# Kernel tuning notes

Hardware: AMD Instinct MI355X
Metric: run time of the kernel (lower is better)

## Reference

```python
import jax, jax.numpy as jnp
import numpy as np

N = 50000      # nodes
E = 800000     # edges
F = 256        # input features (glove identity)
H = 64         # hidden dim of GCN stack
C = 16         # num classes
PE = 200000    # pos/neg edges each

@jax.custom_vjp
def grad_reverse(x):
    return x

def _gr_fwd(x):
    return x, None

def _gr_bwd(_, g):
    return (-g,)

grad_reverse.defvjp(_gr_fwd, _gr_bwd)

def _gcn_norm(edge_index, n):
    # add self loops + symmetric normalization (PyG GCNConv default)
    loops = jnp.arange(n, dtype=edge_index.dtype)
    src = jnp.concatenate([edge_index[0], loops])
    dst = jnp.concatenate([edge_index[1], loops])
    deg = jax.ops.segment_sum(jnp.ones(src.shape, jnp.float32), dst, num_segments=n)
    dinv = jnp.where(deg > 0, jax.lax.rsqrt(jnp.maximum(deg, 1.0)), 0.0)
    return src, dst, dinv[src] * dinv[dst]

def _gcn(x, W, b, src, dst, norm, n):
    h = x @ W                                   # [n, out]
    msg = h[src] * norm[:, None]                # gather + edge scale
    return jax.ops.segment_sum(msg, dst, num_segments=n) + b

def setup_inputs():
    key = jax.random.key(0)
    ks = jax.random.split(key, 14)
    s = 0.05
    return {
        "input": jax.random.normal(ks[0], (N, F), jnp.float32),
        "glove": jnp.eye(F, dtype=jnp.float32),
        "W1": jax.random.normal(ks[1], (F, H), jnp.float32) * s,
        "b1": jnp.zeros((H,), jnp.float32),
        "W2": jax.random.normal(ks[2], (H, H), jnp.float32) * s,
        "b2": jnp.zeros((H,), jnp.float32),
        "W3": jax.random.normal(ks[3], (H, H), jnp.float32) * s,
        "b3": jnp.zeros((H,), jnp.float32),
        "Wa": jax.random.normal(ks[4], (H, C), jnp.float32) * s,
        "ba": jnp.zeros((C,), jnp.float32),
        "Wk": jax.random.normal(ks[5], (H, C), jnp.float32) * s,
        "bk": jnp.zeros((C,), jnp.float32),
        "edge_index": jax.random.randint(ks[6], (2, E), 0, N, dtype=jnp.int32),
        "pos_edge_index": jax.random.randint(ks[7], (2, PE), 0, N, dtype=jnp.int32),
        "neg_edge_index": jax.random.randint(ks[8], (2, PE), 0, N, dtype=jnp.int32),
    }

def reference(input, glove, W1, b1, W2, b2, W3, b3, Wa, ba, Wk, bk,
              edge_index, pos_edge_index, neg_edge_index):
    src, dst, norm = _gcn_norm(edge_index, N)
    x = input @ glove
    x = jax.nn.relu(_gcn(x, W1, b1, src, dst, norm, N))
    x = _gcn(x, W2, b2, src, dst, norm, N)
    x = _gcn(x, W3, b3, src, dst, norm, N)
    feat = x
    attr = _gcn(x, Wa, ba, src, dst, norm, N)
    att = _gcn(grad_reverse(x), Wk, bk, src, dst, norm, N)
    tei = jnp.concatenate([pos_edge_index, neg_edge_index], axis=-1)  # [2, 2*PE]
    x_j = x[tei[0]]
    x_i = x[tei[1]]
    res = jnp.einsum('ef,ef->e', x_i, x_j)
    return res, jax.nn.log_softmax(attr, axis=1), att, feat
```

## Files before the change

### kernel.cpp

```cpp
#include <hip/hip_runtime.h>
#include <hip/hip_bf16.h>

#define N_NODES 50000
#define N_EDGES 800000
#define F_IN    256
#define H_DIM   64
#define C_DIM   16
#define PE_CNT  200000

typedef __hip_bfloat16 bf16;

__device__ __forceinline__ float b2f(bf16 v) { return __bfloat162float(v); }
__device__ __forceinline__ bf16  f2b(float v) { return __float2bfloat16(v); }
__device__ __forceinline__ unsigned short f2b_u(float v) {
    union { bf16 b; unsigned short u; } cv; cv.b = __float2bfloat16(v); return cv.u;
}


__global__ void hist_build_kernel(const int* __restrict__ dst, int* __restrict__ hist,
                                  const float* __restrict__ Wa, const float* __restrict__ Wk,
                                  float* __restrict__ Wh) {
    int e = blockIdx.x * blockDim.x + threadIdx.x;
    if (e < N_EDGES) atomicAdd(&hist[dst[e]], 1);
    if (blockIdx.x == 0) {
        for (int idx = threadIdx.x; idx < H_DIM * 32; idx += 256) {
            int f = idx >> 5, c = idx & 31;
            Wh[idx] = (c < C_DIM) ? Wa[f * C_DIM + c] : Wk[f * C_DIM + (c - C_DIM)];
        }
    }
}

__global__ __launch_bounds__(1024) void scan_block_kernel(const int* __restrict__ hist,
                                                          int* __restrict__ excl,
                                                          int* __restrict__ partials) {
    __shared__ int buf[1024];
    int i = blockIdx.x * 1024 + threadIdx.x;
    int v = (i < N_NODES) ? hist[i] : 0;
    buf[threadIdx.x] = v;
    __syncthreads();
    for (int off = 1; off < 1024; off <<= 1) {
        int t = (threadIdx.x >= off) ? buf[threadIdx.x - off] : 0;
        __syncthreads();
        buf[threadIdx.x] += t;
        __syncthreads();
    }
    int incl = buf[threadIdx.x];
    if (i < N_NODES) excl[i] = incl - v;
    if (threadIdx.x == 1023) partials[blockIdx.x] = incl;
}

__global__ void scan_partials_kernel(int* __restrict__ partials) {
    int t = threadIdx.x;
    int orig = (t < 49) ? partials[t] : 0;
    int v = orig;
    for (int off = 1; off < 64; off <<= 1) {
        int u = __shfl_up(v, off, 64);
        if (t >= off) v += u;
    }
    if (t < 49) partials[t] = v - orig;
}

__global__ void scan_add_kernel(int* __restrict__ rowstart, const int* __restrict__ partials,
                                int* __restrict__ cursor, const int* __restrict__ hist,
                                float* __restrict__ dinv) {
    int i = blockIdx.x * blockDim.x + threadIdx.x;
    if (i < N_NODES) {
        int v = rowstart[i] + partials[i >> 10];
        rowstart[i] = v;
        cursor[i]   = v;
        dinv[i]     = rsqrtf((float)(hist[i] + 1));
    } else if (i == N_NODES) {
        rowstart[i] = N_EDGES;
    }
}

__global__ void scatter_kernel(const int* __restrict__ ei, int* __restrict__ cursor,
                               const float* __restrict__ dinv, int2* __restrict__ csr2) {
    int e = blockIdx.x * blockDim.x + threadIdx.x;
    if (e < N_EDGES) {
        int s = ei[e];
        int d = ei[N_EDGES + e];
        int p = atomicAdd(&cursor[d], 1);
        csr2[p] = make_int2(s, __float_as_int(dinv[s]));
    }
}

#define AGG_BODY(TBL, STRIDE, CIDX)                                                      \
    float acc0 = dn * b2f(TBL[(size_t)node * STRIDE + CIDX]);                            \
    float acc1 = 0.f, acc2 = 0.f, acc3 = 0.f;                                            \
    int j = s0;                                                                          \
    if ((j & 1) && j < s1) {                                                             \
        int2 e = csr2[j];                                                                \
        acc1 += __int_as_float(e.y) * b2f(TBL[(size_t)e.x * STRIDE + CIDX]);             \
        j++;                                                                             \
    }                                                                                    \
    for (; j + 3 < s1; j += 4) {                                                         \
        int4 p01 = *(const int4*)&csr2[j];                                               \
        int4 p23 = *(const int4*)&csr2[j + 2];                                           \
        acc0 += __int_as_float(p01.y) * b2f(TBL[(size_t)p01.x * STRIDE + CIDX]);         \
        acc1 += __int_as_float(p01.w) * b2f(TBL[(size_t)p01.z * STRIDE + CIDX]);         \
        acc2 += __int_as_float(p23.y) * b2f(TBL[(size_t)p23.x * STRIDE + CIDX]);         \
        acc3 += __int_as_float(p23.w) * b2f(TBL[(size_t)p23.z * STRIDE + CIDX]);         \
    }                                                                                    \
    for (; j < s1; j++) {                                                                \
        int2 e = csr2[j];                                                                \
        acc0 += __int_as_float(e.y) * b2f(TBL[(size_t)e.x * STRIDE + CIDX]);             \
    }                                                                                    \
    float aggsum = (acc0 + acc1) + (acc2 + acc3);

#define G_ROWS 32
#define G_KCH  64
#define XS_LD  68

__global__ __launch_bounds__(256) void gemm_k256_kernel(const float* __restrict__ x,
                                                        const float* __restrict__ W,
                                                        bf16* __restrict__ h1) {
    __shared__ float xs[G_ROWS * XS_LD];
    __shared__ float ws[G_KCH * H_DIM];
    int t = threadIdx.x;
    int row0 = blockIdx.x * G_ROWS;
    int c4 = (t & 15) * 4;
    int r2 = (t >> 4) * 2;

    float acc00 = 0.f, acc01 = 0.f, acc02 = 0.f, acc03 = 0.f;
    float acc10 = 0.f, acc11 = 0.f, acc12 = 0.f, acc13 = 0.f;

    for (int c = 0; c < F_IN / G_KCH; c++) {
        int k0 = c * G_KCH;
        {
            const float4* Wg = (const float4*)(W + k0 * H_DIM);
            float4* wl = (float4*)ws;
#pragma unroll
            for (int i = 0; i < 4; i++) wl[t + 256 * i] = Wg[t + 256 * i];
        }
        {
            int r = t >> 3, jj = (t & 7) * 8;
            int row = row0 + r;
            float4 v0 = make_float4(0.f, 0.f, 0.f, 0.f), v1 = v0;
            if (row < N_NODES) {
                const float4* xg = (const float4*)(x + (size_t)row * F_IN + k0 + jj);
                v0 = xg[0];
                v1 = xg[1];
            }
            float4* xl = (float4*)&xs[r * XS_LD + jj];
            xl[0] = v0;
            xl[1] = v1;
        }
        __syncthreads();
#pragma unroll 8
        for (int kk = 0; kk < G_KCH; kk += 4) {
            float4 xv0 = *(const float4*)&xs[(r2 + 0) * XS_LD + kk];
            float4 xv1 = *(const float4*)&xs[(r2 + 1) * XS_LD + kk];
            float4 w0 = *(const float4*)&ws[(kk + 0) * H_DIM + c4];
            float4 w1 = *(const float4*)&ws[(kk + 1) * H_DIM + c4];
            float4 w2 = *(const float4*)&ws[(kk + 2) * H_DIM + c4];
            float4 w3 = *(const float4*)&ws[(kk + 3) * H_DIM + c4];
            acc00 += xv0.x * w0.x + xv0.y * w1.x + xv0.z * w2.x + xv0.w * w3.x;
            acc01 += xv0.x * w0.y + xv0.y * w1.y + xv0.z * w2.y + xv0.w * w3.y;
            acc02 += xv0.x * w0.z + xv0.y * w1.z + xv0.z * w2.z + xv0.w * w3.z;
            acc03 += xv0.x * w0.w + xv0.y * w1.w + xv0.z * w2.w + xv0.w * w3.w;
            acc10 += xv1.x * w0.x + xv1.y * w1.x + xv1.z * w2.x + xv1.w * w3.x;
            acc11 += xv1.x * w0.y + xv1.y * w1.y + xv1.z * w2.y + xv1.w * w3.y;
            acc12 += xv1.x * w0.z + xv1.y * w1.z + xv1.z * w2.z + xv1.w * w3.z;
            acc13 += xv1.x * w0.w + xv1.y * w1.w + xv1.z * w2.w + xv1.w * w3.w;
        }
        __syncthreads();
    }
    int rowA = row0 + r2, rowB = rowA + 1;
    if (rowA < N_NODES) {
        ushort4 p = make_ushort4(f2b_u(acc00), f2b_u(acc01), f2b_u(acc02), f2b_u(acc03));
        *(ushort4*)&h1[(size_t)rowA * H_DIM + c4] = p;
    }
    if (rowB < N_NODES) {
        ushort4 p = make_ushort4(f2b_u(acc10), f2b_u(acc11), f2b_u(acc12), f2b_u(acc13));
        *(ushort4*)&h1[(size_t)rowB * H_DIM + c4] = p;
    }
}

template <int RELU>
__global__ __launch_bounds__(256) void agg_gemm_kernel(const bf16* __restrict__ h,
                                                       const int* __restrict__ rowstart,
                                                       const int2* __restrict__ csr2,
                                                       const float* __restrict__ dinv,
                                                       const float* __restrict__ bagg,
                                                       const float* __restrict__ W,
                                                       bf16* __restrict__ hnext) {
    __shared__ float Wl[H_DIM * H_DIM];
    int t = threadIdx.x;
    {
        const float4* Wg = (const float4*)W;
        float4* wl = (float4*)Wl;
#pragma unroll
        for (int i = 0; i < 4; i++) wl[t + 256 * i] = Wg[t + 256 * i];
    }
    __syncthreads();
    int lane = t & 63;
    int node = blockIdx.x * 4 + __builtin_amdgcn_readfirstlane(t >> 6);
    float dn = dinv[node];
    int s0 = rowstart[node], s1 = rowstart[node + 1];
    AGG_BODY(h, H_DIM, lane)
    float v = dn * aggsum + bagg[lane];
    if (RELU) v = fmaxf(v, 0.f);
    float o = 0.f;
#pragma unroll
    for (int f = 0; f < H_DIM; f++)
        o += __shfl(v, f, 64) * Wl[f * H_DIM + lane];
    hnext[(size_t)node * H_DIM + lane] = f2b(o);
}

__global__ __launch_bounds__(256) void agg_out_kernel(const bf16* __restrict__ h,
                                                      const int* __restrict__ rowstart,
                                                      const int2* __restrict__ csr2,
                                                      const float* __restrict__ dinv,
                                                      const float* __restrict__ b3,
                                                      const float* __restrict__ Wh,
                                                      float* __restrict__ feat,
                                                      bf16* __restrict__ featb,
                                                      bf16* __restrict__ zb) {
    __shared__ float Whs[H_DIM * 32];
    int t = threadIdx.x;
    {
        const float4* Wg = (const float4*)Wh;
        float4* wl = (float4*)Whs;
#pragma unroll
        for (int i = 0; i < 2; i++) wl[t + 256 * i] = Wg[t + 256 * i];
    }
    __syncthreads();
    int lane = t & 63;
    int node = blockIdx.x * 4 + __builtin_amdgcn_readfirstlane(t >> 6);
    float dn = dinv[node];
    int s0 = rowstart[node], s1 = rowstart[node + 1];
    AGG_BODY(h, H_DIM, lane)
    float v = dn * aggsum + b3[lane];
    feat[(size_t)node * H_DIM + lane]  = v;
    featb[(size_t)node * H_DIM + lane] = f2b(v);
    int c32 = lane & 31;
    float zc = 0.f;
#pragma unroll
    for (int f = 0; f < H_DIM; f++)
        zc += __shfl(v, f, 64) * Whs[f * 32 + c32];
    if (lane < 32) zb[(size_t)node * 32 + lane] = f2b(zc);
}

__global__ __launch_bounds__(256) void head_kernel(const bf16* __restrict__ zb,
                                                   const int* __restrict__ rowstart,
                                                   const int2* __restrict__ csr2,
                                                   const float* __restrict__ dinv,
                                                   const float* __restrict__ ba,
                                                   const float* __restrict__ bk,
                                                   float* __restrict__ lsm,
                                                   float* __restrict__ att) {
    int t = threadIdx.x;
    int lane = t & 63;
    int half = lane >> 5;
    int c32 = lane & 31;
    int wid = __builtin_amdgcn_readfirstlane(t >> 6);
    int node = blockIdx.x * 8 + wid * 2 + half;
    float dn = dinv[node];
    int s0 = rowstart[node], s1 = rowstart[node + 1];
    AGG_BODY(zb, 32, c32)
    float y = dn * aggsum;
    int c = c32 & 15;
    float hv = y + ((c32 < 16) ? ba[c] : bk[c]);
    if (c32 < 16) {
        float m = hv;
#pragma unroll
        for (int off = 1; off < 16; off <<= 1) m = fmaxf(m, __shfl_xor(m, off, 64));
        float e = __expf(hv - m);
        float sum = e;
#pragma unroll
        for (int off = 1; off < 16; off <<= 1) sum += __shfl_xor(sum, off, 64);
        lsm[(size_t)node * C_DIM + c] = (hv - m) - __logf(sum);
    } else {
        att[(size_t)node * C_DIM + c] = hv;
    }
}

__global__ __launch_bounds__(256) void edge_dot_kernel(const int* __restrict__ pos,
                                                       const int* __restrict__ neg,
                                                       const bf16* __restrict__ xb,
                                                       float* __restrict__ res) {
    int e = blockIdx.x * 32 + (threadIdx.x >> 3);
    int lane8 = threadIdx.x & 7;
    int a, b;
    if (e < PE_CNT) {
        a = pos[e];
        b = pos[PE_CNT + e];
    } else {
        int e2 = e - PE_CNT;
        a = neg[e2];
        b = neg[PE_CNT + e2];
    }
    uint4 ua = ((const uint4*)(xb + (size_t)a * H_DIM))[lane8];
    uint4 ub = ((const uint4*)(xb + (size_t)b * H_DIM))[lane8];
    float acc;
    {
        float s = 0.f;
        unsigned au, bu;
        au = ua.x; bu = ub.x;
        s += __uint_as_float(au << 16) * __uint_as_float(bu << 16);
        s += __uint_as_float(au & 0xffff0000u) * __uint_as_float(bu & 0xffff0000u);
        au = ua.y; bu = ub.y;
        s += __uint_as_float(au << 16) * __uint_as_float(bu << 16);
        s += __uint_as_float(au & 0xffff0000u) * __uint_as_float(bu & 0xffff0000u);
        au = ua.z; bu = ub.z;
        s += __uint_as_float(au << 16) * __uint_as_float(bu << 16);
        s += __uint_as_float(au & 0xffff0000u) * __uint_as_float(bu & 0xffff0000u);
        au = ua.w; bu = ub.w;
        s += __uint_as_float(au << 16) * __uint_as_float(bu << 16);
        s += __uint_as_float(au & 0xffff0000u) * __uint_as_float(bu & 0xffff0000u);
        acc = s;
    }
#pragma unroll
    for (int off = 1; off < 8; off <<= 1) acc += __shfl_xor(acc, off, 64);
    if (lane8 == 0) res[e] = acc;
}


extern "C" void kernel_launch(void* const* d_in, const int* in_sizes, int n_in,
                              void* d_out, int out_size, void* d_ws, size_t ws_size,
                              hipStream_t stream) {
    const float* input = (const float*)d_in[0];
    const float* W1 = (const float*)d_in[2];
    const float* b1 = (const float*)d_in[3];
    const float* W2 = (const float*)d_in[4];
    const float* b2 = (const float*)d_in[5];
    const float* W3 = (const float*)d_in[6];
    const float* b3 = (const float*)d_in[7];
    const float* Wa = (const float*)d_in[8];
    const float* ba = (const float*)d_in[9];
    const float* Wk = (const float*)d_in[10];
    const float* bk = (const float*)d_in[11];
    const int* ei  = (const int*)d_in[12];
    const int* pos = (const int*)d_in[13];
    const int* neg = (const int*)d_in[14];

    char* ws = (char*)d_ws;
    int*   hist     = (int*)(ws + 0);
    int*   rowstart = (int*)(ws + 200704);
    int*   cursor   = (int*)(ws + 401408);
    float* dinv     = (float*)(ws + 602112);
    int*   partials = (int*)(ws + 802816);
    float* Wh       = (float*)(ws + 803072);
    int2*  csr2     = (int2*)(ws + 811264);
    bf16*  bufA     = (bf16*)(ws + 7211264ULL);
    bf16*  bufB     = (bf16*)(ws + 13611264ULL);
    bf16*  zb       = (bf16*)(ws + 20011264ULL);

    float* out  = (float*)d_out;
    float* res  = out;
    float* lsm  = out + 400000;
    float* att  = out + 1200000;
    float* feat = out + 2000000;

    hipMemsetAsync(hist, 0, N_NODES * sizeof(int), stream);
    hist_build_kernel<<<(N_EDGES + 255) / 256, 256, 0, stream>>>(ei + N_EDGES, hist, Wa, Wk, Wh);
    scan_block_kernel<<<49, 1024, 0, stream>>>(hist, rowstart, partials);
    scan_partials_kernel<<<1, 64, 0, stream>>>(partials);
    scan_add_kernel<<<196, 256, 0, stream>>>(rowstart, partials, cursor, hist, dinv);
    scatter_kernel<<<(N_EDGES + 255) / 256, 256, 0, stream>>>(ei, cursor, dinv, csr2);

    gemm_k256_kernel<<<(N_NODES + G_ROWS - 1) / G_ROWS, 256, 0, stream>>>(input, W1, bufA);
    agg_gemm_kernel<1><<<12500, 256, 0, stream>>>(bufA, rowstart, csr2, dinv, b1, W2, bufB);
    agg_gemm_kernel<0><<<12500, 256, 0, stream>>>(bufB, rowstart, csr2, dinv, b2, W3, bufA);
    agg_out_kernel<<<12500, 256, 0, stream>>>(bufA, rowstart, csr2, dinv, b3, Wh, feat, bufB, zb);
    head_kernel<<<6250, 256, 0, stream>>>(zb, rowstart, csr2, dinv, ba, bk, lsm, att);
    edge_dot_kernel<<<12500, 256, 0, stream>>>(pos, neg, bufB, res);
}
```

Measured before the change: 459.0 us.

## Split CSR by source half to shrink gather working sets for L2 locality

Edges in each destination row are partitioned by source node (low or high half), and each aggregation becomes two passes. The first pass gathers only from the low half of the feature table into an fp32 accumulator buffer, and the second gathers from the high half and finishes the GEMM/epilogue. The edge-dot stage is also split into two passes over 32-column half tables, and the first GEMM uses 64-row tiles. The aim is to keep each pass's random-gather footprint cache resident, at the cost of extra kernel launches, an fp32 partial-sum round trip through memory, and a second read-modify-write of res.

```diff
diff --git a/kernel.cpp b/kernel.cpp
--- a/kernel.cpp
+++ b/kernel.cpp
@@ -2,6 +2,7 @@
 #include <hip/hip_bf16.h>
 
 #define N_NODES 50000
+#define N_HALF  25000
 #define N_EDGES 800000
 #define F_IN    256
 #define H_DIM   64
@@ -17,11 +18,17 @@
 }
 
 
-__global__ void hist_build_kernel(const int* __restrict__ dst, int* __restrict__ hist,
+__global__ void hist_build_kernel(const int* __restrict__ ei, int* __restrict__ hist_tot,
+                                  int* __restrict__ hist_lo,
                                   const float* __restrict__ Wa, const float* __restrict__ Wk,
                                   float* __restrict__ Wh) {
     int e = blockIdx.x * blockDim.x + threadIdx.x;
-    if (e < N_EDGES) atomicAdd(&hist[dst[e]], 1);
+    if (e < N_EDGES) {
+        int s = ei[e];
+        int d = ei[N_EDGES + e];
+        atomicAdd(&hist_tot[d], 1);
+        if (s < N_HALF) atomicAdd(&hist_lo[d], 1);
+    }
     if (blockIdx.x == 0) {
         for (int idx = threadIdx.x; idx < H_DIM * 32; idx += 256) {
             int f = idx >> 5, c = idx & 31;
@@ -61,40 +68,45 @@
 }
 
 __global__ void scan_add_kernel(int* __restrict__ rowstart, const int* __restrict__ partials,
-                                int* __restrict__ cursor, const int* __restrict__ hist,
+                                int* __restrict__ cursorA, int* __restrict__ split,
+                                int* __restrict__ cursorB,
+                                const int* __restrict__ hist_tot, const int* __restrict__ hist_lo,
                                 float* __restrict__ dinv) {
     int i = blockIdx.x * blockDim.x + threadIdx.x;
     if (i < N_NODES) {
         int v = rowstart[i] + partials[i >> 10];
         rowstart[i] = v;
-        cursor[i]   = v;
-        dinv[i]     = rsqrtf((float)(hist[i] + 1));
+        cursorA[i]  = v;
+        int sp = v + hist_lo[i];
+        split[i]    = sp;
+        cursorB[i]  = sp;
+        dinv[i]     = rsqrtf((float)(hist_tot[i] + 1));
     } else if (i == N_NODES) {
         rowstart[i] = N_EDGES;
     }
 }
 
-__global__ void scatter_kernel(const int* __restrict__ ei, int* __restrict__ cursor,
-                               const float* __restrict__ dinv, int2* __restrict__ csr2) {
+__global__ void scatter_kernel(const int* __restrict__ ei, int* __restrict__ cursorA,
+                               int* __restrict__ cursorB, const float* __restrict__ dinv,
+                               int2* __restrict__ csr2) {
     int e = blockIdx.x * blockDim.x + threadIdx.x;
     if (e < N_EDGES) {
         int s = ei[e];
         int d = ei[N_EDGES + e];
-        int p = atomicAdd(&cursor[d], 1);
+        int p = (s < N_HALF) ? atomicAdd(&cursorA[d], 1) : atomicAdd(&cursorB[d], 1);
         csr2[p] = make_int2(s, __float_as_int(dinv[s]));
     }
 }
 
-#define AGG_BODY(TBL, STRIDE, CIDX)                                                      \
-    float acc0 = dn * b2f(TBL[(size_t)node * STRIDE + CIDX]);                            \
+#define AGG_LOOP(TBL, STRIDE, CIDX, J0, J1)                                              \
     float acc1 = 0.f, acc2 = 0.f, acc3 = 0.f;                                            \
-    int j = s0;                                                                          \
-    if ((j & 1) && j < s1) {                                                             \
+    int j = (J0);                                                                        \
+    if ((j & 1) && j < (J1)) {                                                           \
         int2 e = csr2[j];                                                                \
         acc1 += __int_as_float(e.y) * b2f(TBL[(size_t)e.x * STRIDE + CIDX]);             \
         j++;                                                                             \
     }                                                                                    \
-    for (; j + 3 < s1; j += 4) {                                                         \
+    for (; j + 3 < (J1); j += 4) {                                                       \
         int4 p01 = *(const int4*)&csr2[j];                                               \
         int4 p23 = *(const int4*)&csr2[j + 2];                                           \
         acc0 += __int_as_float(p01.y) * b2f(TBL[(size_t)p01.x * STRIDE + CIDX]);         \
@@ -102,13 +114,13 @@
         acc2 += __int_as_float(p23.y) * b2f(TBL[(size_t)p23.x * STRIDE + CIDX]);         \
         acc3 += __int_as_float(p23.w) * b2f(TBL[(size_t)p23.z * STRIDE + CIDX]);         \
     }                                                                                    \
-    for (; j < s1; j++) {                                                                \
+    for (; j < (J1); j++) {                                                              \
         int2 e = csr2[j];                                                                \
         acc0 += __int_as_float(e.y) * b2f(TBL[(size_t)e.x * STRIDE + CIDX]);             \
     }                                                                                    \
     float aggsum = (acc0 + acc1) + (acc2 + acc3);
 
-#define G_ROWS 32
+#define G_ROWS 64
 #define G_KCH  64
 #define XS_LD  68
 
@@ -120,10 +132,13 @@
     int t = threadIdx.x;
     int row0 = blockIdx.x * G_ROWS;
     int c4 = (t & 15) * 4;
-    int r2 = (t >> 4) * 2;
-
-    float acc00 = 0.f, acc01 = 0.f, acc02 = 0.f, acc03 = 0.f;
-    float acc10 = 0.f, acc11 = 0.f, acc12 = 0.f, acc13 = 0.f;
+    int r4 = (t >> 4) * 4;
+
+    float acc[4][4];
+#pragma unroll
+    for (int i = 0; i < 4; i++)
+#pragma unroll
+        for (int q = 0; q < 4; q++) acc[i][q] = 0.f;
 
     for (int c = 0; c < F_IN / G_KCH; c++) {
         int k0 = c * G_KCH;
@@ -134,57 +149,70 @@
             for (int i = 0; i < 4; i++) wl[t + 256 * i] = Wg[t + 256 * i];
         }
         {
-            int r = t >> 3, jj = (t & 7) * 8;
+            int r = t >> 2, jj = (t & 3) * 16;
             int row = row0 + r;
-            float4 v0 = make_float4(0.f, 0.f, 0.f, 0.f), v1 = v0;
+            float4 v0 = make_float4(0.f, 0.f, 0.f, 0.f), v1 = v0, v2 = v0, v3 = v0;
             if (row < N_NODES) {
                 const float4* xg = (const float4*)(x + (size_t)row * F_IN + k0 + jj);
-                v0 = xg[0];
-                v1 = xg[1];
+                v0 = xg[0]; v1 = xg[1]; v2 = xg[2]; v3 = xg[3];
             }
             float4* xl = (float4*)&xs[r * XS_LD + jj];
-            xl[0] = v0;
-            xl[1] = v1;
+            xl[0] = v0; xl[1] = v1; xl[2] = v2; xl[3] = v3;
         }
         __syncthreads();
-#pragma unroll 8
+#pragma unroll 4
         for (int kk = 0; kk < G_KCH; kk += 4) {
-            float4 xv0 = *(const float4*)&xs[(r2 + 0) * XS_LD + kk];
-            float4 xv1 = *(const float4*)&xs[(r2 + 1) * XS_LD + kk];
-            float4 w0 = *(const float4*)&ws[(kk + 0) * H_DIM + c4];
-            float4 w1 = *(const float4*)&ws[(kk + 1) * H_DIM + c4];
-            float4 w2 = *(const float4*)&ws[(kk + 2) * H_DIM + c4];
-            float4 w3 = *(const float4*)&ws[(kk + 3) * H_DIM + c4];
-            acc00 += xv0.x * w0.x + xv0.y * w1.x + xv0.z * w2.x + xv0.w * w3.x;
-            acc01 += xv0.x * w0.y + xv0.y * w1.y + xv0.z * w2.y + xv0.w * w3.y;
-            acc02 += xv0.x * w0.z + xv0.y * w1.z + xv0.z * w2.z + xv0.w * w3.z;
-            acc03 += xv0.x * w0.w + xv0.y * w1.w + xv0.z * w2.w + xv0.w * w3.w;
-            acc10 += xv1.x * w0.x + xv1.y * w1.x + xv1.z * w2.x + xv1.w * w3.x;
-            acc11 += xv1.x * w0.y + xv1.y * w1.y + xv1.z * w2.y + xv1.w * w3.y;
-            acc12 += xv1.x * w0.z + xv1.y * w1.z + xv1.z * w2.z + xv1.w * w3.z;
-            acc13 += xv1.x * w0.w + xv1.y * w1.w + xv1.z * w2.w + xv1.w * w3.w;
+            float4 xv[4], wv[4];
+#pragma unroll
+            for (int i = 0; i < 4; i++) xv[i] = *(const float4*)&xs[(r4 + i) * XS_LD + kk];
+#pragma unroll
+            for (int q = 0; q < 4; q++) wv[q] = *(const float4*)&ws[(kk + q) * H_DIM + c4];
+#pragma unroll
+            for (int i = 0; i < 4; i++) {
+                acc[i][0] += xv[i].x * wv[0].x + xv[i].y * wv[1].x + xv[i].z * wv[2].x + xv[i].w * wv[3].x;
+                acc[i][1] += xv[i].x * wv[0].y + xv[i].y * wv[1].y + xv[i].z * wv[2].y + xv[i].w * wv[3].y;
+                acc[i][2] += xv[i].x * wv[0].z + xv[i].y * wv[1].z + xv[i].z * wv[2].z + xv[i].w * wv[3].z;
+                acc[i][3] += xv[i].x * wv[0].w + xv[i].y * wv[1].w + xv[i].z * wv[2].w + xv[i].w * wv[3].w;
+            }
         }
         __syncthreads();
     }
-    int rowA = row0 + r2, rowB = rowA + 1;
-    if (rowA < N_NODES) {
-        ushort4 p = make_ushort4(f2b_u(acc00), f2b_u(acc01), f2b_u(acc02), f2b_u(acc03));
-        *(ushort4*)&h1[(size_t)rowA * H_DIM + c4] = p;
-    }
-    if (rowB < N_NODES) {
-        ushort4 p = make_ushort4(f2b_u(acc10), f2b_u(acc11), f2b_u(acc12), f2b_u(acc13));
-        *(ushort4*)&h1[(size_t)rowB * H_DIM + c4] = p;
-    }
+#pragma unroll
+    for (int i = 0; i < 4; i++) {
+        int row = row0 + r4 + i;
+        if (row < N_NODES) {
+            ushort4 p = make_ushort4(f2b_u(acc[i][0]), f2b_u(acc[i][1]),
+                                     f2b_u(acc[i][2]), f2b_u(acc[i][3]));
+            *(ushort4*)&h1[(size_t)row * H_DIM + c4] = p;
+        }
+    }
+}
+
+__global__ __launch_bounds__(256) void aggA_kernel(const bf16* __restrict__ h,
+                                                   const int* __restrict__ rowstart,
+                                                   const int* __restrict__ split,
+                                                   const int2* __restrict__ csr2,
+                                                   const float* __restrict__ dinv,
+                                                   float* __restrict__ accbuf) {
+    int lane = threadIdx.x & 63;
+    int node = blockIdx.x * 4 + __builtin_amdgcn_readfirstlane(threadIdx.x >> 6);
+    float dn = dinv[node];
+    int s0 = rowstart[node], s1 = split[node];
+    float acc0 = (node < N_HALF) ? dn * b2f(h[(size_t)node * H_DIM + lane]) : 0.f;
+    AGG_LOOP(h, H_DIM, lane, s0, s1)
+    __builtin_nontemporal_store(aggsum, &accbuf[(size_t)node * H_DIM + lane]);
 }
 
 template <int RELU>
-__global__ __launch_bounds__(256) void agg_gemm_kernel(const bf16* __restrict__ h,
-                                                       const int* __restrict__ rowstart,
-                                                       const int2* __restrict__ csr2,
-                                                       const float* __restrict__ dinv,
-                                                       const float* __restrict__ bagg,
-                                                       const float* __restrict__ W,
-                                                       bf16* __restrict__ hnext) {
+__global__ __launch_bounds__(256) void aggB_gemm_kernel(const bf16* __restrict__ h,
+                                                        const int* __restrict__ rowstart,
+                                                        const int* __restrict__ split,
+                                                        const int2* __restrict__ csr2,
+                                                        const float* __restrict__ dinv,
+                                                        const float* __restrict__ accbuf,
+                                                        const float* __restrict__ bagg,
+                                                        const float* __restrict__ W,
+                                                        bf16* __restrict__ hnext) {
     __shared__ float Wl[H_DIM * H_DIM];
     int t = threadIdx.x;
     {
@@ -197,8 +225,10 @@
     int lane = t & 63;
     int node = blockIdx.x * 4 + __builtin_amdgcn_readfirstlane(t >> 6);
     float dn = dinv[node];
-    int s0 = rowstart[node], s1 = rowstart[node + 1];
-    AGG_BODY(h, H_DIM, lane)
+    int s0 = split[node], s1 = rowstart[node + 1];
+    float acc0 = __builtin_nontemporal_load(&accbuf[(size_t)node * H_DIM + lane]);
+    if (node >= N_HALF) acc0 += dn * b2f(h[(size_t)node * H_DIM + lane]);
+    AGG_LOOP(h, H_DIM, lane, s0, s1)
     float v = dn * aggsum + bagg[lane];
     if (RELU) v = fmaxf(v, 0.f);
     float o = 0.f;
@@ -208,15 +238,18 @@
     hnext[(size_t)node * H_DIM + lane] = f2b(o);
 }
 
-__global__ __launch_bounds__(256) void agg_out_kernel(const bf16* __restrict__ h,
-                                                      const int* __restrict__ rowstart,
-                                                      const int2* __restrict__ csr2,
-                                                      const float* __restrict__ dinv,
-                                                      const float* __restrict__ b3,
-                                                      const float* __restrict__ Wh,
-                                                      float* __restrict__ feat,
-                                                      bf16* __restrict__ featb,
-                                                      bf16* __restrict__ zb) {
+__global__ __launch_bounds__(256) void aggB_out_kernel(const bf16* __restrict__ h,
+                                                       const int* __restrict__ rowstart,
+                                                       const int* __restrict__ split,
+                                                       const int2* __restrict__ csr2,
+                                                       const float* __restrict__ dinv,
+                                                       const float* __restrict__ accbuf,
+                                                       const float* __restrict__ b3,
+                                                       const float* __restrict__ Wh,
+                                                       float* __restrict__ feat,
+                                                       bf16* __restrict__ featL,
+                                                       bf16* __restrict__ featH,
+                                                       bf16* __restrict__ zb) {
     __shared__ float Whs[H_DIM * 32];
     int t = threadIdx.x;
     {
@@ -229,12 +262,15 @@
     int lane = t & 63;
     int node = blockIdx.x * 4 + __builtin_amdgcn_readfirstlane(t >> 6);
     float dn = dinv[node];
-    int s0 = rowstart[node], s1 = rowstart[node + 1];
-    AGG_BODY(h, H_DIM, lane)
+    int s0 = split[node], s1 = rowstart[node + 1];
+    float acc0 = __builtin_nontemporal_load(&accbuf[(size_t)node * H_DIM + lane]);
+    if (node >= N_HALF) acc0 += dn * b2f(h[(size_t)node * H_DIM + lane]);
+    AGG_LOOP(h, H_DIM, lane, s0, s1)
     float v = dn * aggsum + b3[lane];
-    feat[(size_t)node * H_DIM + lane]  = v;
-    featb[(size_t)node * H_DIM + lane] = f2b(v);
+    feat[(size_t)node * H_DIM + lane] = v;
     int c32 = lane & 31;
+    bf16* half_tbl = (lane >= 32) ? featH : featL;
+    half_tbl[(size_t)node * 32 + c32] = f2b(v);
     float zc = 0.f;
 #pragma unroll
     for (int f = 0; f < H_DIM; f++)
@@ -258,7 +294,8 @@
     int node = blockIdx.x * 8 + wid * 2 + half;
     float dn = dinv[node];
     int s0 = rowstart[node], s1 = rowstart[node + 1];
-    AGG_BODY(zb, 32, c32)
+    float acc0 = dn * b2f(zb[(size_t)node * 32 + c32]);
+    AGG_LOOP(zb, 32, c32, s0, s1)
     float y = dn * aggsum;
     int c = c32 & 15;
     float hv = y + ((c32 < 16) ? ba[c] : bk[c]);
@@ -278,10 +315,11 @@
 
 __global__ __launch_bounds__(256) void edge_dot_kernel(const int* __restrict__ pos,
                                                        const int* __restrict__ neg,
-                                                       const bf16* __restrict__ xb,
-                                                       float* __restrict__ res) {
-    int e = blockIdx.x * 32 + (threadIdx.x >> 3);
-    int lane8 = threadIdx.x & 7;
+                                                       const bf16* __restrict__ tbl,
+                                                       float* __restrict__ res,
+                                                       int accumulate) {
+    int e = blockIdx.x * 64 + (threadIdx.x >> 2);
+    int lane4 = threadIdx.x & 3;
     int a, b;
     if (e < PE_CNT) {
         a = pos[e];
@@ -291,29 +329,28 @@
         a = neg[e2];
         b = neg[PE_CNT + e2];
     }
-    uint4 ua = ((const uint4*)(xb + (size_t)a * H_DIM))[lane8];
-    uint4 ub = ((const uint4*)(xb + (size_t)b * H_DIM))[lane8];
-    float acc;
-    {
-        float s = 0.f;
-        unsigned au, bu;
-        au = ua.x; bu = ub.x;
-        s += __uint_as_float(au << 16) * __uint_as_float(bu << 16);
-        s += __uint_as_float(au & 0xffff0000u) * __uint_as_float(bu & 0xffff0000u);
-        au = ua.y; bu = ub.y;
-        s += __uint_as_float(au << 16) * __uint_as_float(bu << 16);
-        s += __uint_as_float(au & 0xffff0000u) * __uint_as_float(bu & 0xffff0000u);
-        au = ua.z; bu = ub.z;
-        s += __uint_as_float(au << 16) * __uint_as_float(bu << 16);
-        s += __uint_as_float(au & 0xffff0000u) * __uint_as_float(bu & 0xffff0000u);
-        au = ua.w; bu = ub.w;
-        s += __uint_as_float(au << 16) * __uint_as_float(bu << 16);
-        s += __uint_as_float(au & 0xffff0000u) * __uint_as_float(bu & 0xffff0000u);
-        acc = s;
-    }
-#pragma unroll
-    for (int off = 1; off < 8; off <<= 1) acc += __shfl_xor(acc, off, 64);
-    if (lane8 == 0) res[e] = acc;
+    uint4 ua = ((const uint4*)(tbl + (size_t)a * 32))[lane4];
+    uint4 ub = ((const uint4*)(tbl + (size_t)b * 32))[lane4];
+    float s = 0.f;
+    unsigned au, bu;
+    au = ua.x; bu = ub.x;
+    s += __uint_as_float(au << 16) * __uint_as_float(bu << 16);
+    s += __uint_as_float(au & 0xffff0000u) * __uint_as_float(bu & 0xffff0000u);
+    au = ua.y; bu = ub.y;
+    s += __uint_as_float(au << 16) * __uint_as_float(bu << 16);
+    s += __uint_as_float(au & 0xffff0000u) * __uint_as_float(bu & 0xffff0000u);
+    au = ua.z; bu = ub.z;
+    s += __uint_as_float(au << 16) * __uint_as_float(bu << 16);
+    s += __uint_as_float(au & 0xffff0000u) * __uint_as_float(bu & 0xffff0000u);
+    au = ua.w; bu = ub.w;
+    s += __uint_as_float(au << 16) * __uint_as_float(bu << 16);
+    s += __uint_as_float(au & 0xffff0000u) * __uint_as_float(bu & 0xffff0000u);
+#pragma unroll
+    for (int off = 1; off < 4; off <<= 1) s += __shfl_xor(s, off, 64);
+    if (lane4 == 0) {
+        if (accumulate) res[e] += s;
+        else            res[e]  = s;
+    }
 }
 
 
@@ -336,16 +373,22 @@
     const int* neg = (const int*)d_in[14];
 
     char* ws = (char*)d_ws;
-    int*   hist     = (int*)(ws + 0);
-    int*   rowstart = (int*)(ws + 200704);
-    int*   cursor   = (int*)(ws + 401408);
-    float* dinv     = (float*)(ws + 602112);
-    int*   partials = (int*)(ws + 802816);
-    float* Wh       = (float*)(ws + 803072);
-    int2*  csr2     = (int2*)(ws + 811264);
-    bf16*  bufA     = (bf16*)(ws + 7211264ULL);
-    bf16*  bufB     = (bf16*)(ws + 13611264ULL);
-    bf16*  zb       = (bf16*)(ws + 20011264ULL);
+    int*   hist_tot = (int*)(ws + 0);
+    int*   hist_lo  = (int*)(ws + 200704);
+    int*   rowstart = (int*)(ws + 401408);
+    int*   cursorA  = (int*)(ws + 602112);
+    int*   split    = (int*)(ws + 802816);
+    int*   cursorB  = (int*)(ws + 1003520);
+    float* dinv     = (float*)(ws + 1204224);
+    int*   partials = (int*)(ws + 1404928);
+    float* Wh       = (float*)(ws + 1405184);
+    int2*  csr2     = (int2*)(ws + 1413376);
+    bf16*  bufA     = (bf16*)(ws + 7813376ULL);
+    bf16*  bufB     = (bf16*)(ws + 14213376ULL);
+    bf16*  zb       = (bf16*)(ws + 20613376ULL);
+    bf16*  featL    = (bf16*)(ws + 23813376ULL);
+    bf16*  featH    = (bf16*)(ws + 27013376ULL);
+    float* accbuf   = (float*)(ws + 30213376ULL);
 
     float* out  = (float*)d_out;
     float* res  = out;
@@ -353,17 +396,26 @@
     float* att  = out + 1200000;
     float* feat = out + 2000000;
 
-    hipMemsetAsync(hist, 0, N_NODES * sizeof(int), stream);
-    hist_build_kernel<<<(N_EDGES + 255) / 256, 256, 0, stream>>>(ei + N_EDGES, hist, Wa, Wk, Wh);
-    scan_block_kernel<<<49, 1024, 0, stream>>>(hist, rowstart, partials);
+    hipMemsetAsync(hist_tot, 0, 401408, stream);
+    hist_build_kernel<<<3125, 256, 0, stream>>>(ei, hist_tot, hist_lo, Wa, Wk, Wh);
+    scan_block_kernel<<<49, 1024, 0, stream>>>(hist_tot, rowstart, partials);
     scan_partials_kernel<<<1, 64, 0, stream>>>(partials);
-    scan_add_kernel<<<196, 256, 0, stream>>>(rowstart, partials, cursor, hist, dinv);
-    scatter_kernel<<<(N_EDGES + 255) / 256, 256, 0, stream>>>(ei, cursor, dinv, csr2);
+    scan_add_kernel<<<196, 256, 0, stream>>>(rowstart, partials, cursorA, split, cursorB,
+                                             hist_tot, hist_lo, dinv);
+    scatter_kernel<<<3125, 256, 0, stream>>>(ei, cursorA, cursorB, dinv, csr2);
 
     gemm_k256_kernel<<<(N_NODES + G_ROWS - 1) / G_ROWS, 256, 0, stream>>>(input, W1, bufA);
-    agg_gemm_kernel<1><<<12500, 256, 0, stream>>>(bufA, rowstart, csr2, dinv, b1, W2, bufB);
-    agg_gemm_kernel<0><<<12500, 256, 0, stream>>>(bufB, rowstart, csr2, dinv, b2, W3, bufA);
-    agg_out_kernel<<<12500, 256, 0, stream>>>(bufA, rowstart, csr2, dinv, b3, Wh, feat, bufB, zb);
+
+    aggA_kernel<<<12500, 256, 0, stream>>>(bufA, rowstart, split, csr2, dinv, accbuf);
+    aggB_gemm_kernel<1><<<12500, 256, 0, stream>>>(bufA, rowstart, split, csr2, dinv,
+                                                   accbuf, b1, W2, bufB);
+    aggA_kernel<<<12500, 256, 0, stream>>>(bufB, rowstart, split, csr2, dinv, accbuf);
+    aggB_gemm_kernel<0><<<12500, 256, 0, stream>>>(bufB, rowstart, split, csr2, dinv,
+                                                   accbuf, b2, W3, bufA);
+    aggA_kernel<<<12500, 256, 0, stream>>>(bufA, rowstart, split, csr2, dinv, accbuf);
+    aggB_out_kernel<<<12500, 256, 0, stream>>>(bufA, rowstart, split, csr2, dinv,
+                                               accbuf, b3, Wh, feat, featL, featH, zb);
     head_kernel<<<6250, 256, 0, stream>>>(zb, rowstart, csr2, dinv, ba, bk, lsm, att);
-    edge_dot_kernel<<<12500, 256, 0, stream>>>(pos, neg, bufB, res);
-}
+    edge_dot_kernel<<<6250, 256, 0, stream>>>(pos, neg, featL, res, 0);
+    edge_dot_kernel<<<6250, 256, 0, stream>>>(pos, neg, featH, res, 1);
+}
```

After: 520.1 us. +13.3%, slower.
